# Kernel optimization log

Measured on AMD Instinct MI355X. Metric: run time of the kernel, lower is better.

The kernel has to match this reference:

```python
import jax, jax.numpy as jnp
import numpy as np

B, N, E = 4, 20000, 320000
IN_DIM, HID, OUT = 64, 128, 16


def setup_inputs() -> dict:
    key = jax.random.key(0)
    ks = jax.random.split(key, 10)
    return {
        "graph_nodes": jax.random.normal(ks[0], (B, N, IN_DIM), jnp.float32),
        "additional_features": jax.random.normal(ks[1], (B, 1), jnp.float32),
        "edge_index": jax.random.randint(ks[2], (2, E), 0, N, dtype=jnp.int32).astype(jnp.int64),
        "W1": jax.random.normal(ks[3], (IN_DIM, HID), jnp.float32) / np.sqrt(IN_DIM),
        "b1": jnp.zeros((HID,), jnp.float32),
        "W2": jax.random.normal(ks[4], (HID, HID), jnp.float32) / np.sqrt(HID),
        "b2": jnp.zeros((HID,), jnp.float32),
        "fc_w": jax.random.normal(ks[5], (HID + 1, OUT), jnp.float32) / np.sqrt(HID + 1),
        "fc_b": jnp.zeros((OUT,), jnp.float32),
        "sigma_param": jnp.zeros((OUT, 1), jnp.float32),
    }


def gcn_conv(x, src, dst, W, b, n):
    # PyG GCNConv: h = x @ W; out[dst] += deg^-1/2[src]*deg^-1/2[dst] * h[src]; out += b
    h = x @ W  # [B, N, H]
    deg = jnp.zeros((n,), h.dtype).at[dst].add(jnp.ones(dst.shape[0], h.dtype))
    dis = jax.lax.rsqrt(deg)  # self-loops guarantee deg >= 1
    norm = dis[src] * dis[dst]  # [E+N]
    msg = h[:, src, :] * norm[None, :, None]  # [B, E+N, H]
    out = jnp.zeros_like(h).at[:, dst, :].add(msg)
    return out + b


def reference(graph_nodes, additional_features, W1, b1, W2, b2, fc_w, fc_b, sigma_param, edge_index):
    n = graph_nodes.shape[1]
    loops = jnp.arange(n, dtype=edge_index.dtype)  # add_self_loops
    src = jnp.concatenate([edge_index[0], loops])
    dst = jnp.concatenate([edge_index[1], loops])
    x = jax.nn.relu(gcn_conv(graph_nodes, src, dst, W1, b1, n))
    x = jax.nn.relu(gcn_conv(x, src, dst, W2, b2, n))
    pooled = x.mean(axis=1)  # global_mean_pool (equal-size graphs)
    feats = jnp.concatenate([pooled, additional_features], axis=1)  # [B, HID+1]
    mu = feats @ fc_w + fc_b  # [B, OUT]
    sigma = jnp.exp(jnp.broadcast_to(sigma_param.reshape(1, -1), mu.shape))
    return mu, sigma
```

## Files before the change

kernel.cpp:

```cpp
#include <hip/hip_runtime.h>
#include <math.h>

#define HID 128
#define INDIM 64
#define NSH 64

typedef unsigned int uint;
typedef unsigned short ushort;
typedef __attribute__((ext_vector_type(8))) short short8;
typedef __attribute__((ext_vector_type(4))) float f32x4;

static __device__ inline float bf2f(uint h) { return __uint_as_float(h << 16); }
static __device__ inline ushort f2bf(float f) {
    uint u = __float_as_uint(f);
    return (ushort)((u + 0x7fff + ((u >> 16) & 1)) >> 16);
}
static __device__ inline uint packbf2(float a, float b) {
    return (uint)f2bf(a) | ((uint)f2bf(b) << 16);
}
static __device__ inline int imin(int a, int b) { return a < b ? a : b; }

static __device__ inline void init4(float* a, uint2 v, float sl) {
    a[0] = bf2f(v.x & 0xffffu) * sl; a[1] = bf2f(v.x >> 16) * sl;
    a[2] = bf2f(v.y & 0xffffu) * sl; a[3] = bf2f(v.y >> 16) * sl;
}
static __device__ inline void acc4(float* a, uint2 u, float f) {
    a[0] = fmaf(bf2f(u.x & 0xffffu), f, a[0]); a[1] = fmaf(bf2f(u.x >> 16), f, a[1]);
    a[2] = fmaf(bf2f(u.y & 0xffffu), f, a[2]); a[3] = fmaf(bf2f(u.y >> 16), f, a[3]);
}

__global__ __launch_bounds__(256) void k_init_cast(
    const float* __restrict__ x, const float* __restrict__ W1, const float* __restrict__ W2,
    const int* __restrict__ ei,
    uint* __restrict__ xbf, uint* __restrict__ w1t, uint* __restrict__ w2t,
    int* cnt, float* pooledS, int* flag, int N)
{
    int gid = blockIdx.x * 256 + threadIdx.x;
    int stride = gridDim.x * 256;
    if (blockIdx.x == 0) {
        __shared__ int sbad;
        if (threadIdx.x == 0) sbad = 0;
        __syncthreads();
        int bad = (ei[2 * threadIdx.x + 1] != 0) ? 1 : 0;
        if (__any(bad) && (threadIdx.x & 63) == 0) atomicOr(&sbad, 1);
        __syncthreads();
        if (threadIdx.x == 0) *flag = sbad;
    }
    int total = N * 128;
    for (int i = gid; i < total; i += stride) {
        int n = i >> 7, r = i & 127;
        int b = r >> 5, c2 = r & 31;
        const float* s = x + ((size_t)b * N + n) * 64 + c2 * 2;
        xbf[i] = packbf2(s[0], s[1]);
    }
    if (gid < 128 * 32) { int c = gid >> 5, k2 = gid & 31; w1t[gid] = packbf2(W1[(2 * k2) * 128 + c], W1[(2 * k2 + 1) * 128 + c]); }
    if (gid < 128 * 64) { int c = gid >> 6, k2 = gid & 63; w2t[gid] = packbf2(W2[(2 * k2) * 128 + c], W2[(2 * k2 + 1) * 128 + c]); }
    if (gid < N) cnt[gid] = 0;
    if (gid < NSH * 512) pooledS[gid] = 0.f;
}

__global__ __launch_bounds__(256) void k_edges(const int* __restrict__ ei, const int* __restrict__ flag,
                                               int* __restrict__ src, int* __restrict__ dst,
                                               int* cnt, int E) {
    int e = blockIdx.x * 256 + threadIdx.x;
    if (e >= E) return;
    int s, d;
    if (*flag) { s = ei[e]; d = ei[(size_t)E + e]; }
    else       { s = ei[2 * (size_t)e]; d = ei[2 * (size_t)E + 2 * (size_t)e]; }
    src[e] = s; dst[e] = d;
    atomicAdd(&cnt[d], 1);
}

__global__ __launch_bounds__(1024) void k_scan(const int* __restrict__ cnt, int* __restrict__ row_ptr,
                                               float* __restrict__ dis, int* __restrict__ fillcnt, int N) {
    __shared__ int wsum[16];
    int t = threadIdx.x;
    int chunk = (N + 1023) >> 10;
    int lo = t * chunk; if (lo > N) lo = N;
    int hi = lo + chunk; if (hi > N) hi = N;
    int s = 0;
#pragma unroll 4
    for (int i = lo; i < hi; i++) s += cnt[i];
    int lane = t & 63, wid = t >> 6;
    int v = s;
#pragma unroll
    for (int d = 1; d < 64; d <<= 1) {
        int u = __shfl_up(v, d);
        if (lane >= d) v += u;
    }
    if (lane == 63) wsum[wid] = v;
    __syncthreads();
    if (wid == 0) {
        int wv = (lane < 16) ? wsum[lane] : 0;
#pragma unroll
        for (int d = 1; d < 16; d <<= 1) {
            int u = __shfl_up(wv, d);
            if (lane >= d) wv += u;
        }
        if (lane < 16) wsum[lane] = wv;
    }
    __syncthreads();
    int base = (wid > 0 ? wsum[wid - 1] : 0) + (v - s);
    int acc = base;
#pragma unroll 4
    for (int i = lo; i < hi; i++) {
        row_ptr[i] = acc;
        int c = cnt[i];
        acc += c;
        dis[i] = rsqrtf((float)(c + 1));
        fillcnt[i] = 0;
    }
    if (t == 0) row_ptr[N] = wsum[15];
}

__global__ __launch_bounds__(256) void k_fill(const int* __restrict__ src, const int* __restrict__ dst,
                                              const int* __restrict__ row_ptr, int* fillcnt,
                                              int* __restrict__ col, float* __restrict__ wsrc,
                                              const float* __restrict__ dis, int E) {
    int e = blockIdx.x * 256 + threadIdx.x;
    if (e >= E) return;
    int d = dst[e], s = src[e];
    int p = row_ptr[d] + atomicAdd(&fillcnt[d], 1);
    col[p] = s;
    wsrc[p] = dis[s];
}

__global__ __launch_bounds__(256, 4) void k_l1(
    const uint* __restrict__ xbf, const int* __restrict__ rp, const int* __restrict__ col,
    const float* __restrict__ wsrc, const float* __restrict__ dis,
    const uint* __restrict__ w1t, const float* __restrict__ b1,
    uint* __restrict__ x1, int ntile)
{
    __shared__ __align__(16) char sW[16384];
    __shared__ __align__(16) char sXa[4][2048];
    int t = threadIdx.x, w = t >> 6, l = t & 63;
    int g = l >> 4, row = l & 15;
    for (int i = t; i < 1024; i += 256) {
        int c = i >> 3, ch = i & 7;
        *(uint4*)(sW + c * 128 + ((ch ^ (c & 7)) << 4)) = *(const uint4*)(w1t + c * 32 + ch * 4);
    }
    __syncthreads();
    int tile = blockIdx.x * 4 + w;
    if (tile >= ntile) return;
    char* sX = sXa[w];
    const uint2* xr = (const uint2*)xbf;

    int n0 = tile * 4;
    int r0 = rp[n0], r1 = rp[n0 + 1], r2 = rp[n0 + 2], r3 = rp[n0 + 3], r4 = rp[n0 + 4];
    int e0 = r0, e1 = r1, e2 = r2, e3 = r3;
    float dn0 = dis[n0], dn1 = dis[n0 + 1], dn2 = dis[n0 + 2], dn3 = dis[n0 + 3];
    float ac0[4], ac1[4], ac2[4], ac3[4];
    init4(ac0, xr[(size_t)n0 * 64 + l], dn0 * dn0);
    init4(ac1, xr[(size_t)(n0 + 1) * 64 + l], dn1 * dn1);
    init4(ac2, xr[(size_t)(n0 + 2) * 64 + l], dn2 * dn2);
    init4(ac3, xr[(size_t)(n0 + 3) * 64 + l], dn3 * dn3);

#define A2(j) do { \
    int c0_ = col[e##j], c1_ = col[e##j + 1]; \
    float f0_ = wsrc[e##j] * dn##j, f1_ = wsrc[e##j + 1] * dn##j; \
    uint2 u0_ = xr[(size_t)c0_ * 64 + l], u1_ = xr[(size_t)c1_ * 64 + l]; \
    acc4(ac##j, u0_, f0_); acc4(ac##j, u1_, f1_); e##j += 2; } while (0)
#define A1(j) do { \
    int c0_ = col[e##j]; float f0_ = wsrc[e##j] * dn##j; \
    uint2 u0_ = xr[(size_t)c0_ * 64 + l]; acc4(ac##j, u0_, f0_); e##j += 1; } while (0)

    int m = imin(imin(r1 - e0, r2 - e1), imin(r3 - e2, r4 - e3)) >> 1;
    for (int it = 0; it < m; it++) { A2(0); A2(1); A2(2); A2(3); }
    int p01 = imin(r1 - e0, r2 - e1) >> 1;
    for (int it = 0; it < p01; it++) { A2(0); A2(1); }
    int p23 = imin(r3 - e2, r4 - e3) >> 1;
    for (int it = 0; it < p23; it++) { A2(2); A2(3); }
    while (e0 + 1 < r1) A2(0);
    if (e0 < r1) A1(0);
    while (e1 + 1 < r2) A2(1);
    if (e1 < r2) A1(1);
    while (e2 + 1 < r3) A2(2);
    if (e2 < r3) A1(2);
    while (e3 + 1 < r4) A2(3);
    if (e3 < r4) A1(3);
#undef A2
#undef A1

    {
        uint2 pk;
        pk.x = packbf2(ac0[0], ac0[1]); pk.y = packbf2(ac0[2], ac0[3]);
        int wr = g;
        *(uint2*)(sX + wr * 128 + (((row >> 1) ^ (wr & 7)) << 4) + ((row & 1) << 3)) = pk;
        pk.x = packbf2(ac1[0], ac1[1]); pk.y = packbf2(ac1[2], ac1[3]);
        wr = 4 + g;
        *(uint2*)(sX + wr * 128 + (((row >> 1) ^ (wr & 7)) << 4) + ((row & 1) << 3)) = pk;
        pk.x = packbf2(ac2[0], ac2[1]); pk.y = packbf2(ac2[2], ac2[3]);
        wr = 8 + g;
        *(uint2*)(sX + wr * 128 + (((row >> 1) ^ (wr & 7)) << 4) + ((row & 1) << 3)) = pk;
        pk.x = packbf2(ac3[0], ac3[1]); pk.y = packbf2(ac3[2], ac3[3]);
        wr = 12 + g;
        *(uint2*)(sX + wr * 128 + (((row >> 1) ^ (wr & 7)) << 4) + ((row & 1) << 3)) = pk;
    }
    int ro0 = row * 128 + ((g ^ (row & 7)) << 4);
    int ro1 = row * 128 + (((4 + g) ^ (row & 7)) << 4);
    short8 xf0 = *(const short8*)(sX + ro0);
    short8 xf1 = *(const short8*)(sX + ro1);
    size_t rbase = ((size_t)tile * 16 + row) * 32;
#pragma unroll
    for (int q = 0; q < 8; q++) {
        f32x4 a = {0.f, 0.f, 0.f, 0.f};
        const char* wb = sW + q * 2048;
        a = __builtin_amdgcn_mfma_f32_16x16x32_bf16(*(const short8*)(wb + ro0), xf0, a, 0, 0, 0);
        a = __builtin_amdgcn_mfma_f32_16x16x32_bf16(*(const short8*)(wb + ro1), xf1, a, 0, 0, 0);
        float4 bb = *(const float4*)(b1 + q * 16 + g * 4);
        uint2 o;
        o.x = packbf2(fmaxf(a.x + bb.x, 0.f), fmaxf(a.y + bb.y, 0.f));
        o.y = packbf2(fmaxf(a.z + bb.z, 0.f), fmaxf(a.w + bb.w, 0.f));
        ((uint2*)x1)[rbase + q * 4 + g] = o;
    }
}

__global__ __launch_bounds__(256) void k_l2(
    const uint* __restrict__ x1, const int* __restrict__ rp, const int* __restrict__ col,
    const float* __restrict__ wsrc, const float* __restrict__ dis,
    const ushort* __restrict__ w2t, const float* __restrict__ b2,
    float* __restrict__ pooledS, int ntile, float invN)
{
    __shared__ __align__(16) char sX[2 * 4096];
    int t = threadIdx.x, w = t >> 6, l = t & 63;
    int g = l >> 4, row = l & 15;
    int ct0 = 2 * w, ct1 = 2 * w + 1;
    short8 wf0[4], wf1[4];
#pragma unroll
    for (int ks = 0; ks < 4; ks++) {
        wf0[ks] = *(const short8*)(w2t + (ct0 * 16 + row) * 128 + ks * 32 + g * 8);
        wf1[ks] = *(const short8*)(w2t + (ct1 * 16 + row) * 128 + ks * 32 + g * 8);
    }
    float4 bb0 = *(const float4*)(b2 + ct0 * 16 + g * 4);
    float4 bb1 = *(const float4*)(b2 + ct1 * 16 + g * 4);
    int wrow = w * 4 + g;
    int woff = wrow * 256 + (((row) ^ (wrow & 7)) << 4);
    int roff[4];
#pragma unroll
    for (int ks = 0; ks < 4; ks++) roff[ks] = row * 256 + (((ks * 4 + g) ^ (row & 7)) << 4);
    const uint4* xr = (const uint4*)x1;
    float p0[4] = {0.f, 0.f, 0.f, 0.f}, p1[4] = {0.f, 0.f, 0.f, 0.f};

    int it = 0;
    for (int tile = blockIdx.x; tile < ntile; tile += gridDim.x, it++) {
        int n = tile * 4 + w;
        float dn = dis[n];
        int beg = rp[n], end = rp[n + 1];
        uint4 v = xr[(size_t)n * 64 + l];
        float sl = dn * dn;
        float a0 = bf2f(v.x & 0xffffu) * sl, a1 = bf2f(v.x >> 16) * sl;
        float a2 = bf2f(v.y & 0xffffu) * sl, a3 = bf2f(v.y >> 16) * sl;
        float a4 = bf2f(v.z & 0xffffu) * sl, a5 = bf2f(v.z >> 16) * sl;
        float a6 = bf2f(v.w & 0xffffu) * sl, a7 = bf2f(v.w >> 16) * sl;
        int e = beg;
        for (; e + 3 < end; e += 4) {
            int s0 = col[e], s1 = col[e + 1], s2 = col[e + 2], s3 = col[e + 3];
            float f0 = wsrc[e] * dn, f1 = wsrc[e + 1] * dn;
            float f2 = wsrc[e + 2] * dn, f3 = wsrc[e + 3] * dn;
            uint4 u0 = xr[(size_t)s0 * 64 + l], u1 = xr[(size_t)s1 * 64 + l];
            uint4 u2 = xr[(size_t)s2 * 64 + l], u3 = xr[(size_t)s3 * 64 + l];
            a0 = fmaf(bf2f(u0.x & 0xffffu), f0, a0); a1 = fmaf(bf2f(u0.x >> 16), f0, a1);
            a2 = fmaf(bf2f(u0.y & 0xffffu), f0, a2); a3 = fmaf(bf2f(u0.y >> 16), f0, a3);
            a4 = fmaf(bf2f(u0.z & 0xffffu), f0, a4); a5 = fmaf(bf2f(u0.z >> 16), f0, a5);
            a6 = fmaf(bf2f(u0.w & 0xffffu), f0, a6); a7 = fmaf(bf2f(u0.w >> 16), f0, a7);
            a0 = fmaf(bf2f(u1.x & 0xffffu), f1, a0); a1 = fmaf(bf2f(u1.x >> 16), f1, a1);
            a2 = fmaf(bf2f(u1.y & 0xffffu), f1, a2); a3 = fmaf(bf2f(u1.y >> 16), f1, a3);
            a4 = fmaf(bf2f(u1.z & 0xffffu), f1, a4); a5 = fmaf(bf2f(u1.z >> 16), f1, a5);
            a6 = fmaf(bf2f(u1.w & 0xffffu), f1, a6); a7 = fmaf(bf2f(u1.w >> 16), f1, a7);
            a0 = fmaf(bf2f(u2.x & 0xffffu), f2, a0); a1 = fmaf(bf2f(u2.x >> 16), f2, a1);
            a2 = fmaf(bf2f(u2.y & 0xffffu), f2, a2); a3 = fmaf(bf2f(u2.y >> 16), f2, a3);
            a4 = fmaf(bf2f(u2.z & 0xffffu), f2, a4); a5 = fmaf(bf2f(u2.z >> 16), f2, a5);
            a6 = fmaf(bf2f(u2.w & 0xffffu), f2, a6); a7 = fmaf(bf2f(u2.w >> 16), f2, a7);
            a0 = fmaf(bf2f(u3.x & 0xffffu), f3, a0); a1 = fmaf(bf2f(u3.x >> 16), f3, a1);
            a2 = fmaf(bf2f(u3.y & 0xffffu), f3, a2); a3 = fmaf(bf2f(u3.y >> 16), f3, a3);
            a4 = fmaf(bf2f(u3.z & 0xffffu), f3, a4); a5 = fmaf(bf2f(u3.z >> 16), f3, a5);
            a6 = fmaf(bf2f(u3.w & 0xffffu), f3, a6); a7 = fmaf(bf2f(u3.w >> 16), f3, a7);
        }
        for (; e < end; e++) {
            int s = col[e];
            float f = wsrc[e] * dn;
            uint4 u = xr[(size_t)s * 64 + l];
            a0 = fmaf(bf2f(u.x & 0xffffu), f, a0); a1 = fmaf(bf2f(u.x >> 16), f, a1);
            a2 = fmaf(bf2f(u.y & 0xffffu), f, a2); a3 = fmaf(bf2f(u.y >> 16), f, a3);
            a4 = fmaf(bf2f(u.z & 0xffffu), f, a4); a5 = fmaf(bf2f(u.z >> 16), f, a5);
            a6 = fmaf(bf2f(u.w & 0xffffu), f, a6); a7 = fmaf(bf2f(u.w >> 16), f, a7);
        }
        char* wb = sX + (it & 1) * 4096;
        uint4 pk;
        pk.x = packbf2(a0, a1); pk.y = packbf2(a2, a3);
        pk.z = packbf2(a4, a5); pk.w = packbf2(a6, a7);
        *(uint4*)(wb + woff) = pk;
        __syncthreads();
        short8 xf[4];
#pragma unroll
        for (int ks = 0; ks < 4; ks++) xf[ks] = *(const short8*)(wb + roff[ks]);
        f32x4 acc0 = {0.f, 0.f, 0.f, 0.f}, acc1 = {0.f, 0.f, 0.f, 0.f};
#pragma unroll
        for (int ks = 0; ks < 4; ks++) {
            acc0 = __builtin_amdgcn_mfma_f32_16x16x32_bf16(wf0[ks], xf[ks], acc0, 0, 0, 0);
            acc1 = __builtin_amdgcn_mfma_f32_16x16x32_bf16(wf1[ks], xf[ks], acc1, 0, 0, 0);
        }
        p0[0] += fmaxf(acc0.x + bb0.x, 0.f); p0[1] += fmaxf(acc0.y + bb0.y, 0.f);
        p0[2] += fmaxf(acc0.z + bb0.z, 0.f); p0[3] += fmaxf(acc0.w + bb0.w, 0.f);
        p1[0] += fmaxf(acc1.x + bb1.x, 0.f); p1[1] += fmaxf(acc1.y + bb1.y, 0.f);
        p1[2] += fmaxf(acc1.z + bb1.z, 0.f); p1[3] += fmaxf(acc1.w + bb1.w, 0.f);
    }
#pragma unroll
    for (int i = 0; i < 4; i++) {
        p0[i] += __shfl_xor(p0[i], 4); p0[i] += __shfl_xor(p0[i], 8);
        p1[i] += __shfl_xor(p1[i], 4); p1[i] += __shfl_xor(p1[i], 8);
    }
    if ((l & 12) == 0) {
        int b = l & 3;
        float* pd = pooledS + (size_t)(blockIdx.x & (NSH - 1)) * 512 + b * 128;
#pragma unroll
        for (int i = 0; i < 4; i++) {
            atomicAdd(&pd[ct0 * 16 + g * 4 + i], p0[i] * invN);
            atomicAdd(&pd[ct1 * 16 + g * 4 + i], p1[i] * invN);
        }
    }
}

__global__ __launch_bounds__(512) void k_head(const float* __restrict__ pooledS, const float* __restrict__ af,
                                              const float* __restrict__ fcw, const float* __restrict__ fcb,
                                              const float* __restrict__ sig, float* __restrict__ out, int B) {
    __shared__ float pool[512];
    int t = threadIdx.x;
    float s = 0.f;
#pragma unroll 8
    for (int sh = 0; sh < NSH; sh++) s += pooledS[sh * 512 + t];
    pool[t] = s;
    __syncthreads();
    if (t >= B * 16) return;
    int b = t >> 4, o = t & 15;
    float acc = fcb[o];
    for (int c = 0; c < HID; c++) acc = fmaf(pool[b * 128 + c], fcw[c * 16 + o], acc);
    acc = fmaf(af[b], fcw[HID * 16 + o], acc);
    out[t] = acc;
    out[B * 16 + t] = expf(sig[o]);
}


extern "C" void kernel_launch(void* const* d_in, const int* in_sizes, int n_in,
                              void* d_out, int out_size, void* d_ws, size_t ws_size,
                              hipStream_t stream) {
    const float* x   = (const float*)d_in[0];
    const float* af  = (const float*)d_in[1];
    const int*   ei  = (const int*)d_in[2];
    const float* W1  = (const float*)d_in[3];
    const float* b1  = (const float*)d_in[4];
    const float* W2  = (const float*)d_in[5];
    const float* b2  = (const float*)d_in[6];
    const float* fcw = (const float*)d_in[7];
    const float* fcb = (const float*)d_in[8];
    const float* sig = (const float*)d_in[9];

    int B = in_sizes[1];
    int E = in_sizes[2] / 2;
    int N = in_sizes[0] / (B * INDIM);
    int ntile = N / 4;

    char* p = (char*)d_ws;
    auto alloc = [&](size_t bytes) { void* r = (void*)p; p += (bytes + 255) & ~(size_t)255; return r; };
    int*    cnt     = (int*)alloc((size_t)N * 4);
    int*    fillcnt = (int*)alloc((size_t)N * 4);
    int*    row_ptr = (int*)alloc((size_t)(N + 1) * 4);
    int*    colA    = (int*)alloc((size_t)E * 4);
    int*    srcA    = (int*)alloc((size_t)E * 4);
    int*    dstA    = (int*)alloc((size_t)E * 4);
    float*  wsrcA   = (float*)alloc((size_t)E * 4);
    float*  dis     = (float*)alloc((size_t)N * 4);
    float*  pooledS = (float*)alloc((size_t)NSH * 512 * 4);
    int*    flag    = (int*)alloc(256);
    uint*   xbf     = (uint*)alloc((size_t)N * 128 * 4);
    uint*   x1      = (uint*)alloc((size_t)N * 4 * 64 * 4);
    uint*   w1t     = (uint*)alloc((size_t)128 * 32 * 4);
    uint*   w2t     = (uint*)alloc((size_t)128 * 64 * 4);
    (void)ws_size;

    int gE = (E + 255) / 256;
    int gL1 = (ntile + 3) / 4;

    k_init_cast<<<2048, 256, 0, stream>>>(x, W1, W2, ei, xbf, w1t, w2t, cnt, pooledS, flag, N);
    k_edges<<<gE, 256, 0, stream>>>(ei, flag, srcA, dstA, cnt, E);
    k_scan<<<1, 1024, 0, stream>>>(cnt, row_ptr, dis, fillcnt, N);
    k_fill<<<gE, 256, 0, stream>>>(srcA, dstA, row_ptr, fillcnt, colA, wsrcA, dis, E);

    k_l1<<<gL1, 256, 0, stream>>>(xbf, row_ptr, colA, wsrcA, dis, w1t, b1, x1, ntile);
    k_l2<<<2048, 256, 0, stream>>>(x1, row_ptr, colA, wsrcA, dis, (const ushort*)w2t, b2, pooledS, ntile, 1.0f / (float)N);

    k_head<<<1, 512, 0, stream>>>(pooledS, af, fcw, fcb, sig, (float*)d_out, B);
}
```

Before: 156.6 us.

## Store layer-1 output batch-major and gather per batch in layer-2 with 16-node tiles

Layer 1 now writes its bf16 activations in a batch-major [B][N][128] layout instead of node-interleaved across batches. Layer 2 maps each block to a single batch through an interleaved block-to-batch mapping, so each wave gathers 256-byte rows per neighbour, aggregates 16 nodes into LDS, then runs the W2 MFMA with weights read from global memory. The aim is a smaller per-gather footprint and better L2 locality per batch slice, with fewer block-wide barriers. The cost is four times as many gather instructions per edge (one per batch), plus more shuffle reductions and atomics per tile.

```diff
diff --git a/kernel.cpp b/kernel.cpp
--- a/kernel.cpp
+++ b/kernel.cpp
@@ -129,7 +129,7 @@
     const uint* __restrict__ xbf, const int* __restrict__ rp, const int* __restrict__ col,
     const float* __restrict__ wsrc, const float* __restrict__ dis,
     const uint* __restrict__ w1t, const float* __restrict__ b1,
-    uint* __restrict__ x1, int ntile)
+    uint* __restrict__ x1, int N, int ntile)
 {
     __shared__ __align__(16) char sW[16384];
     __shared__ __align__(16) char sXa[4][2048];
@@ -200,123 +200,101 @@
     int ro1 = row * 128 + (((4 + g) ^ (row & 7)) << 4);
     short8 xf0 = *(const short8*)(sX + ro0);
     short8 xf1 = *(const short8*)(sX + ro1);
-    size_t rbase = ((size_t)tile * 16 + row) * 32;
+    int nodeL = row >> 2, bb = row & 3;
+    size_t rnew = ((size_t)bb * N + (size_t)tile * 4 + nodeL) * 32;
 #pragma unroll
     for (int q = 0; q < 8; q++) {
         f32x4 a = {0.f, 0.f, 0.f, 0.f};
         const char* wb = sW + q * 2048;
         a = __builtin_amdgcn_mfma_f32_16x16x32_bf16(*(const short8*)(wb + ro0), xf0, a, 0, 0, 0);
         a = __builtin_amdgcn_mfma_f32_16x16x32_bf16(*(const short8*)(wb + ro1), xf1, a, 0, 0, 0);
-        float4 bb = *(const float4*)(b1 + q * 16 + g * 4);
+        float4 bbv = *(const float4*)(b1 + q * 16 + g * 4);
         uint2 o;
-        o.x = packbf2(fmaxf(a.x + bb.x, 0.f), fmaxf(a.y + bb.y, 0.f));
-        o.y = packbf2(fmaxf(a.z + bb.z, 0.f), fmaxf(a.w + bb.w, 0.f));
-        ((uint2*)x1)[rbase + q * 4 + g] = o;
-    }
-}
-
-__global__ __launch_bounds__(256) void k_l2(
+        o.x = packbf2(fmaxf(a.x + bbv.x, 0.f), fmaxf(a.y + bbv.y, 0.f));
+        o.y = packbf2(fmaxf(a.z + bbv.z, 0.f), fmaxf(a.w + bbv.w, 0.f));
+        ((uint2*)x1)[rnew + q * 4 + g] = o;
+    }
+}
+
+#define BATCH_MAP() \
+    int bid = blockIdx.x; \
+    int bq = (bid & 7) >> 1; \
+    int jj = ((bid >> 3) << 1) | (bid & 1); \
+    int tl = jj * 4 + w; \
+    if (tl >= ntiles) return;
+
+__global__ __launch_bounds__(256, 6) void k_l2(
     const uint* __restrict__ x1, const int* __restrict__ rp, const int* __restrict__ col,
     const float* __restrict__ wsrc, const float* __restrict__ dis,
-    const ushort* __restrict__ w2t, const float* __restrict__ b2,
-    float* __restrict__ pooledS, int ntile, float invN)
+    const uint* __restrict__ w2t, const float* __restrict__ b2,
+    float* __restrict__ pooledS, int N, int ntiles, float invN)
 {
-    __shared__ __align__(16) char sX[2 * 4096];
+    __shared__ __align__(16) char sXa[4][4096];
     int t = threadIdx.x, w = t >> 6, l = t & 63;
     int g = l >> 4, row = l & 15;
-    int ct0 = 2 * w, ct1 = 2 * w + 1;
-    short8 wf0[4], wf1[4];
-#pragma unroll
-    for (int ks = 0; ks < 4; ks++) {
-        wf0[ks] = *(const short8*)(w2t + (ct0 * 16 + row) * 128 + ks * 32 + g * 8);
-        wf1[ks] = *(const short8*)(w2t + (ct1 * 16 + row) * 128 + ks * 32 + g * 8);
-    }
-    float4 bb0 = *(const float4*)(b2 + ct0 * 16 + g * 4);
-    float4 bb1 = *(const float4*)(b2 + ct1 * 16 + g * 4);
-    int wrow = w * 4 + g;
-    int woff = wrow * 256 + (((row) ^ (wrow & 7)) << 4);
-    int roff[4];
-#pragma unroll
-    for (int ks = 0; ks < 4; ks++) roff[ks] = row * 256 + (((ks * 4 + g) ^ (row & 7)) << 4);
-    const uint4* xr = (const uint4*)x1;
-    float p0[4] = {0.f, 0.f, 0.f, 0.f}, p1[4] = {0.f, 0.f, 0.f, 0.f};
-
-    int it = 0;
-    for (int tile = blockIdx.x; tile < ntile; tile += gridDim.x, it++) {
-        int n = tile * 4 + w;
-        float dn = dis[n];
-        int beg = rp[n], end = rp[n + 1];
-        uint4 v = xr[(size_t)n * 64 + l];
+    BATCH_MAP();
+    char* sX = sXa[w];
+    const uint* xb = x1 + (size_t)bq * N * 64;
+    int n0 = tl * 16;
+    int lofs = (((l >> 2) ^ 99) & 0);  (void)lofs;
+
+    for (int p = 0; p < 16; p++) {
+        int node = n0 + p;
+        float dn = dis[node];
+        int beg = rp[node], end = rp[node + 1];
+        uint v = xb[(size_t)node * 64 + l];
         float sl = dn * dn;
-        float a0 = bf2f(v.x & 0xffffu) * sl, a1 = bf2f(v.x >> 16) * sl;
-        float a2 = bf2f(v.y & 0xffffu) * sl, a3 = bf2f(v.y >> 16) * sl;
-        float a4 = bf2f(v.z & 0xffffu) * sl, a5 = bf2f(v.z >> 16) * sl;
-        float a6 = bf2f(v.w & 0xffffu) * sl, a7 = bf2f(v.w >> 16) * sl;
+        float a0 = bf2f(v & 0xffffu) * sl, a1 = bf2f(v >> 16) * sl;
         int e = beg;
         for (; e + 3 < end; e += 4) {
             int s0 = col[e], s1 = col[e + 1], s2 = col[e + 2], s3 = col[e + 3];
             float f0 = wsrc[e] * dn, f1 = wsrc[e + 1] * dn;
             float f2 = wsrc[e + 2] * dn, f3 = wsrc[e + 3] * dn;
-            uint4 u0 = xr[(size_t)s0 * 64 + l], u1 = xr[(size_t)s1 * 64 + l];
-            uint4 u2 = xr[(size_t)s2 * 64 + l], u3 = xr[(size_t)s3 * 64 + l];
-            a0 = fmaf(bf2f(u0.x & 0xffffu), f0, a0); a1 = fmaf(bf2f(u0.x >> 16), f0, a1);
-            a2 = fmaf(bf2f(u0.y & 0xffffu), f0, a2); a3 = fmaf(bf2f(u0.y >> 16), f0, a3);
-            a4 = fmaf(bf2f(u0.z & 0xffffu), f0, a4); a5 = fmaf(bf2f(u0.z >> 16), f0, a5);
-            a6 = fmaf(bf2f(u0.w & 0xffffu), f0, a6); a7 = fmaf(bf2f(u0.w >> 16), f0, a7);
-            a0 = fmaf(bf2f(u1.x & 0xffffu), f1, a0); a1 = fmaf(bf2f(u1.x >> 16), f1, a1);
-            a2 = fmaf(bf2f(u1.y & 0xffffu), f1, a2); a3 = fmaf(bf2f(u1.y >> 16), f1, a3);
-            a4 = fmaf(bf2f(u1.z & 0xffffu), f1, a4); a5 = fmaf(bf2f(u1.z >> 16), f1, a5);
-            a6 = fmaf(bf2f(u1.w & 0xffffu), f1, a6); a7 = fmaf(bf2f(u1.w >> 16), f1, a7);
-            a0 = fmaf(bf2f(u2.x & 0xffffu), f2, a0); a1 = fmaf(bf2f(u2.x >> 16), f2, a1);
-            a2 = fmaf(bf2f(u2.y & 0xffffu), f2, a2); a3 = fmaf(bf2f(u2.y >> 16), f2, a3);
-            a4 = fmaf(bf2f(u2.z & 0xffffu), f2, a4); a5 = fmaf(bf2f(u2.z >> 16), f2, a5);
-            a6 = fmaf(bf2f(u2.w & 0xffffu), f2, a6); a7 = fmaf(bf2f(u2.w >> 16), f2, a7);
-            a0 = fmaf(bf2f(u3.x & 0xffffu), f3, a0); a1 = fmaf(bf2f(u3.x >> 16), f3, a1);
-            a2 = fmaf(bf2f(u3.y & 0xffffu), f3, a2); a3 = fmaf(bf2f(u3.y >> 16), f3, a3);
-            a4 = fmaf(bf2f(u3.z & 0xffffu), f3, a4); a5 = fmaf(bf2f(u3.z >> 16), f3, a5);
-            a6 = fmaf(bf2f(u3.w & 0xffffu), f3, a6); a7 = fmaf(bf2f(u3.w >> 16), f3, a7);
+            uint u0 = xb[(size_t)s0 * 64 + l];
+            uint u1 = xb[(size_t)s1 * 64 + l];
+            uint u2 = xb[(size_t)s2 * 64 + l];
+            uint u3 = xb[(size_t)s3 * 64 + l];
+            a0 = fmaf(bf2f(u0 & 0xffffu), f0, a0); a1 = fmaf(bf2f(u0 >> 16), f0, a1);
+            a0 = fmaf(bf2f(u1 & 0xffffu), f1, a0); a1 = fmaf(bf2f(u1 >> 16), f1, a1);
+            a0 = fmaf(bf2f(u2 & 0xffffu), f2, a0); a1 = fmaf(bf2f(u2 >> 16), f2, a1);
+            a0 = fmaf(bf2f(u3 & 0xffffu), f3, a0); a1 = fmaf(bf2f(u3 >> 16), f3, a1);
         }
         for (; e < end; e++) {
             int s = col[e];
             float f = wsrc[e] * dn;
-            uint4 u = xr[(size_t)s * 64 + l];
-            a0 = fmaf(bf2f(u.x & 0xffffu), f, a0); a1 = fmaf(bf2f(u.x >> 16), f, a1);
-            a2 = fmaf(bf2f(u.y & 0xffffu), f, a2); a3 = fmaf(bf2f(u.y >> 16), f, a3);
-            a4 = fmaf(bf2f(u.z & 0xffffu), f, a4); a5 = fmaf(bf2f(u.z >> 16), f, a5);
-            a6 = fmaf(bf2f(u.w & 0xffffu), f, a6); a7 = fmaf(bf2f(u.w >> 16), f, a7);
+            uint u = xb[(size_t)s * 64 + l];
+            a0 = fmaf(bf2f(u & 0xffffu), f, a0); a1 = fmaf(bf2f(u >> 16), f, a1);
         }
-        char* wb = sX + (it & 1) * 4096;
-        uint4 pk;
-        pk.x = packbf2(a0, a1); pk.y = packbf2(a2, a3);
-        pk.z = packbf2(a4, a5); pk.w = packbf2(a6, a7);
-        *(uint4*)(wb + woff) = pk;
-        __syncthreads();
-        short8 xf[4];
+        *(uint*)(sX + p * 256 + ((((l >> 2) ^ (p & 7))) << 4) + ((l & 3) << 2)) = packbf2(a0, a1);
+    }
+    short8 xf[4];
 #pragma unroll
-        for (int ks = 0; ks < 4; ks++) xf[ks] = *(const short8*)(wb + roff[ks]);
-        f32x4 acc0 = {0.f, 0.f, 0.f, 0.f}, acc1 = {0.f, 0.f, 0.f, 0.f};
-#pragma unroll
-        for (int ks = 0; ks < 4; ks++) {
-            acc0 = __builtin_amdgcn_mfma_f32_16x16x32_bf16(wf0[ks], xf[ks], acc0, 0, 0, 0);
-            acc1 = __builtin_amdgcn_mfma_f32_16x16x32_bf16(wf1[ks], xf[ks], acc1, 0, 0, 0);
-        }
-        p0[0] += fmaxf(acc0.x + bb0.x, 0.f); p0[1] += fmaxf(acc0.y + bb0.y, 0.f);
-        p0[2] += fmaxf(acc0.z + bb0.z, 0.f); p0[3] += fmaxf(acc0.w + bb0.w, 0.f);
-        p1[0] += fmaxf(acc1.x + bb1.x, 0.f); p1[1] += fmaxf(acc1.y + bb1.y, 0.f);
-        p1[2] += fmaxf(acc1.z + bb1.z, 0.f); p1[3] += fmaxf(acc1.w + bb1.w, 0.f);
-    }
-#pragma unroll
-    for (int i = 0; i < 4; i++) {
-        p0[i] += __shfl_xor(p0[i], 4); p0[i] += __shfl_xor(p0[i], 8);
-        p1[i] += __shfl_xor(p1[i], 4); p1[i] += __shfl_xor(p1[i], 8);
-    }
-    if ((l & 12) == 0) {
-        int b = l & 3;
-        float* pd = pooledS + (size_t)(blockIdx.x & (NSH - 1)) * 512 + b * 128;
-#pragma unroll
-        for (int i = 0; i < 4; i++) {
-            atomicAdd(&pd[ct0 * 16 + g * 4 + i], p0[i] * invN);
-            atomicAdd(&pd[ct1 * 16 + g * 4 + i], p1[i] * invN);
+    for (int ks = 0; ks < 4; ks++)
+        xf[ks] = *(const short8*)(sX + row * 256 + (((ks * 4 + g) ^ (row & 7)) << 4));
+    int sh = tl & (NSH - 1);
+    float* pd = pooledS + (size_t)sh * 512 + bq * 128;
+#pragma unroll 2
+    for (int q = 0; q < 8; q++) {
+        const uint* wq = w2t + (q * 16 + row) * 64 + g * 4;
+        f32x4 a = {0.f, 0.f, 0.f, 0.f};
+        a = __builtin_amdgcn_mfma_f32_16x16x32_bf16(*(const short8*)(wq),      xf[0], a, 0, 0, 0);
+        a = __builtin_amdgcn_mfma_f32_16x16x32_bf16(*(const short8*)(wq + 16), xf[1], a, 0, 0, 0);
+        a = __builtin_amdgcn_mfma_f32_16x16x32_bf16(*(const short8*)(wq + 32), xf[2], a, 0, 0, 0);
+        a = __builtin_amdgcn_mfma_f32_16x16x32_bf16(*(const short8*)(wq + 48), xf[3], a, 0, 0, 0);
+        float4 bb = *(const float4*)(b2 + q * 16 + g * 4);
+        float v0 = fmaxf(a.x + bb.x, 0.f);
+        float v1 = fmaxf(a.y + bb.y, 0.f);
+        float v2 = fmaxf(a.z + bb.z, 0.f);
+        float v3 = fmaxf(a.w + bb.w, 0.f);
+        v0 += __shfl_xor(v0, 1); v0 += __shfl_xor(v0, 2); v0 += __shfl_xor(v0, 4); v0 += __shfl_xor(v0, 8);
+        v1 += __shfl_xor(v1, 1); v1 += __shfl_xor(v1, 2); v1 += __shfl_xor(v1, 4); v1 += __shfl_xor(v1, 8);
+        v2 += __shfl_xor(v2, 1); v2 += __shfl_xor(v2, 2); v2 += __shfl_xor(v2, 4); v2 += __shfl_xor(v2, 8);
+        v3 += __shfl_xor(v3, 1); v3 += __shfl_xor(v3, 2); v3 += __shfl_xor(v3, 4); v3 += __shfl_xor(v3, 8);
+        if (row == 0) {
+            atomicAdd(&pd[q * 16 + g * 4 + 0], v0 * invN);
+            atomicAdd(&pd[q * 16 + g * 4 + 1], v1 * invN);
+            atomicAdd(&pd[q * 16 + g * 4 + 2], v2 * invN);
+            atomicAdd(&pd[q * 16 + g * 4 + 3], v3 * invN);
         }
     }
 }
@@ -358,7 +336,8 @@
     int B = in_sizes[1];
     int E = in_sizes[2] / 2;
     int N = in_sizes[0] / (B * INDIM);
-    int ntile = N / 4;
+    int ntile1 = N / 4;
+    int ntiles2 = N / 16;
 
     char* p = (char*)d_ws;
     auto alloc = [&](size_t bytes) { void* r = (void*)p; p += (bytes + 255) & ~(size_t)255; return r; };
@@ -379,15 +358,16 @@
     (void)ws_size;
 
     int gE = (E + 255) / 256;
-    int gL1 = (ntile + 3) / 4;
+    int gL1 = (ntile1 + 3) / 4;
+    int gL2 = 8 * ((((ntiles2 + 3) / 4) + 1) / 2);
 
     k_init_cast<<<2048, 256, 0, stream>>>(x, W1, W2, ei, xbf, w1t, w2t, cnt, pooledS, flag, N);
     k_edges<<<gE, 256, 0, stream>>>(ei, flag, srcA, dstA, cnt, E);
     k_scan<<<1, 1024, 0, stream>>>(cnt, row_ptr, dis, fillcnt, N);
     k_fill<<<gE, 256, 0, stream>>>(srcA, dstA, row_ptr, fillcnt, colA, wsrcA, dis, E);
 
-    k_l1<<<gL1, 256, 0, stream>>>(xbf, row_ptr, colA, wsrcA, dis, w1t, b1, x1, ntile);
-    k_l2<<<2048, 256, 0, stream>>>(x1, row_ptr, colA, wsrcA, dis, (const ushort*)w2t, b2, pooledS, ntile, 1.0f / (float)N);
+    k_l1<<<gL1, 256, 0, stream>>>(xbf, row_ptr, colA, wsrcA, dis, w1t, b1, x1, N, ntile1);
+    k_l2<<<gL2, 256, 0, stream>>>(x1, row_ptr, colA, wsrcA, dis, w2t, b2, pooledS, N, ntiles2, 1.0f / (float)N);
 
     k_head<<<1, 512, 0, stream>>>(pooledS, af, fcw, fcb, sig, (float*)d_out, B);
 }
```

Result: slower. 190.4 us (+21.6%).
